# Kernel optimization log

Measured on AMD Instinct MI355X. Metric: run time of the kernel, lower is better.

Reference implementation:

```python
import jax, jax.numpy as jnp
import numpy as np

B, D, F = 64, 256, 64   # batch, in_features (window), feat_num (nodes per graph)
H, C = 4, 64            # heads, out_features per head
OUT = 64                # final out_features after concat projection
NEG_SLOPE = 0.2


def _build_edges():
    # fully connected minus self-loops within each graph, batched with node offsets
    ii = np.repeat(np.arange(F), F)
    jj = np.tile(np.arange(F), F)
    m = ii != jj
    es, ed = ii[m], jj[m]                       # [E0], E0 = F*(F-1)
    off = (np.arange(B) * F)[:, None]
    src = (es[None, :] + off).reshape(-1)       # [B*E0]
    dst = (ed[None, :] + off).reshape(-1)
    return jnp.asarray(src, jnp.int32), jnp.asarray(dst, jnp.int32)


def setup_inputs() -> dict:
    key = jax.random.key(0)
    ks = jax.random.split(key, 6)
    x = jax.random.normal(ks[0], (B, D, F), dtype=jnp.float32)
    s = 1.0 / np.sqrt(D)
    Wl = jax.random.normal(ks[1], (D, H * C), dtype=jnp.float32) * s
    Wr = jax.random.normal(ks[2], (D, H * C), dtype=jnp.float32) * s
    att = jax.random.normal(ks[3], (H, C), dtype=jnp.float32) * (1.0 / np.sqrt(C))
    bias = jax.random.normal(ks[4], (H * C,), dtype=jnp.float32) * 0.02
    Wlin = jax.random.normal(ks[5], (OUT, H * C), dtype=jnp.float32) * (1.0 / np.sqrt(H * C))
    src, dst = _build_edges()
    return {"x": x, "Wl": Wl, "Wr": Wr, "att": att, "bias": bias, "Wlin": Wlin,
            "src": src, "dst": dst}


def reference(x, Wl, Wr, att, bias, Wlin, src, dst):
    N = B * F
    xn = x.transpose(0, 2, 1).reshape(N, D)              # [N, D] node features
    xl = (xn @ Wl).reshape(N, H, C)                      # source transform
    xr = (xn @ Wr).reshape(N, H, C)                      # target transform
    # GATv2 edge scores: a^T LeakyReLU(xl[src] + xr[dst])
    e = jnp.einsum('ehc,hc->eh',
                   jax.nn.leaky_relu(xl[src] + xr[dst], NEG_SLOPE), att)  # [E, H]
    # segment softmax over incoming edges of each destination node
    emax = jax.ops.segment_max(e, dst, num_segments=N)   # [N, H]
    ee = jnp.exp(e - emax[dst])
    denom = jax.ops.segment_sum(ee, dst, num_segments=N)
    alpha = ee / denom[dst]                              # [E, H]
    # weighted scatter-aggregate of source messages
    agg = jax.ops.segment_sum(alpha[:, :, None] * xl[src], dst, num_segments=N)  # [N, H, C]
    out = agg.reshape(N, H * C) + bias
    out = out @ Wlin.T                                   # concat -> OUT projection
    return out.reshape(B, F, OUT).transpose(0, 2, 1)     # [B, OUT, F]
```

## Files before the change

### kernel.cpp

```cpp
#include <hip/hip_runtime.h>
#include <math.h>

#define B_   64
#define D_   256
#define F_   64
#define H_   4
#define C_   64
#define OUT_ 64
#define HC   256
#define N_   4096

typedef __attribute__((ext_vector_type(8)))  short bf16x8;
typedef __attribute__((ext_vector_type(16))) float f32x16;

static __device__ __forceinline__ unsigned short f2bf(float f) {
    unsigned int u = __float_as_uint(f);
    u += 0x7FFFu + ((u >> 16) & 1u);
    return (unsigned short)(u >> 16);
}
static __device__ __forceinline__ float bf2f(unsigned short h) {
    return __uint_as_float(((unsigned int)h) << 16);
}

#define GLDS(g, l) __builtin_amdgcn_global_load_lds(                         \
    (const __attribute__((address_space(1))) unsigned int*)(g),              \
    (__attribute__((address_space(3))) unsigned int*)(l), 16, 0, 0)

__global__ __launch_bounds__(256) void p0_split(
    const float* __restrict__ x, const float* __restrict__ Wl,
    const float* __restrict__ Wr,
    unsigned short* __restrict__ AThi, unsigned short* __restrict__ ATlo,
    unsigned short* __restrict__ WThi, unsigned short* __restrict__ WTlo,
    float* __restrict__ outz)
{
    __shared__ float T[128 * 65];
    const int t = threadIdx.x, blk = blockIdx.x;

    if (blk >= 144) {
        const int zb = blk - 144;
        float4* dst = (float4*)(outz + (size_t)zb * 16384);
        const float4 z = make_float4(0.f, 0.f, 0.f, 0.f);
        #pragma unroll
        for (int i = 0; i < 16; ++i) dst[i * 256 + t] = z;
        return;
    }

    const float* src; int sstride, k0, rowbase;
    unsigned short *Dhi, *Dlo;
    if (blk < 128) {
        int b = blk >> 1, kq = blk & 1;
        src = x + (size_t)b * (D_ * F_) + (size_t)(kq * 128) * F_;
        sstride = F_; k0 = kq * 128; rowbase = b * 64;
        Dhi = AThi; Dlo = ATlo;
    } else {
        int wi = blk - 128;
        int wsel = wi >> 3, rr = wi & 7, jc = rr >> 1, kq = rr & 1;
        src = (wsel ? Wr : Wl) + (size_t)(kq * 128) * HC + jc * 64;
        sstride = HC; k0 = kq * 128; rowbase = wsel * 256 + jc * 64;
        Dhi = WThi; Dlo = WTlo;
    }
    #pragma unroll
    for (int r = 0; r < 8; ++r) {
        int idx = r * 256 + t;
        int kk = idx >> 4, c4 = (idx & 15) * 4;
        float4 v = *(const float4*)&src[(size_t)kk * sstride + c4];
        T[kk * 65 + c4 + 0] = v.x;
        T[kk * 65 + c4 + 1] = v.y;
        T[kk * 65 + c4 + 2] = v.z;
        T[kk * 65 + c4 + 3] = v.w;
    }
    __syncthreads();
    const int c = t & 63, kg = t >> 6;
    const int row = rowbase + c;
    for (int cc = 0; cc < 4; ++cc) {
        int cg   = (k0 >> 3) + kg * 4 + cc;
        int phys = cg ^ (row & 7);
        unsigned int ph[4], pl[4];
        #pragma unroll
        for (int j = 0; j < 4; ++j) {
            float v0 = T[(kg * 32 + cc * 8 + 2 * j + 0) * 65 + c];
            float v1 = T[(kg * 32 + cc * 8 + 2 * j + 1) * 65 + c];
            unsigned short h0 = f2bf(v0), h1 = f2bf(v1);
            unsigned short l0 = f2bf(v0 - bf2f(h0)), l1 = f2bf(v1 - bf2f(h1));
            ph[j] = (unsigned int)h0 | ((unsigned int)h1 << 16);
            pl[j] = (unsigned int)l0 | ((unsigned int)l1 << 16);
        }
        *(uint4*)&Dhi[(size_t)row * 256 + phys * 8] = make_uint4(ph[0], ph[1], ph[2], ph[3]);
        *(uint4*)&Dlo[(size_t)row * 256 + phys * 8] = make_uint4(pl[0], pl[1], pl[2], pl[3]);
    }
}

__global__ __launch_bounds__(512, 2) void fused(
    const unsigned short* __restrict__ AThi, const unsigned short* __restrict__ ATlo,
    const unsigned short* __restrict__ WThi, const unsigned short* __restrict__ WTlo,
    const float* __restrict__ att, const float* __restrict__ bias,
    const float* __restrict__ Wlin, float* __restrict__ out)
{
    __shared__ __align__(16) char smem[98304];
    unsigned short* Ah = (unsigned short*)smem;
    unsigned short* Al = Ah + 64 * 128;
    unsigned short* Bh = Al + 64 * 128;
    unsigned short* Bl = Bh + 128 * 128;
    float* XL   = (float*)smem;
    float* XR   = XL + 64 * 68;
    float* ATe  = XR + 64 * 68;
    float* SUMD = ATe + 64 * 65;
    float* AGG  = SUMD + 64;
    float* WC   = AGG + 64 * 65;

    const int t = threadIdx.x;
    const int h = blockIdx.x, b = blockIdx.y;
    const int lane = t & 63, wid = t >> 6;
    const int wm = wid & 1, wn = wid >> 1;
    const int kg = lane >> 5, m = lane & 31;

    f32x16 acc = {};
    for (int kt = 0; kt < 2; ++kt) {
        for (int i = 0; i < 12; ++i) {
            int q = wid * 12 + i;
            const unsigned short* P; unsigned short* Lb; int li;
            if (q < 16)      { P = AThi; Lb = Ah; li = q; }
            else if (q < 32) { P = ATlo; Lb = Al; li = q - 16; }
            else if (q < 64) { P = WThi; Lb = Bh; li = q - 32; }
            else             { P = WTlo; Lb = Bl; li = q - 64; }
            int gi = li * 64 + lane;
            int row = gi >> 4, cl = gi & 15;
            int prow;
            if (q < 32) prow = b * 64 + row;
            else        prow = (row < 64) ? (h * 64 + row) : (256 + h * 64 + row - 64);
            GLDS(P + (size_t)prow * 256 + (size_t)(kt * 16 + cl) * 8, Lb + li * 512);
        }
        __syncthreads();

        const int rA = wm * 32 + m;
        const int rB = wn * 32 + m;
        #pragma unroll
        for (int s = 0; s < 8; ++s) {
            int pA = (2 * s + kg) ^ (rA & 7);
            bf16x8 ah = *(const bf16x8*)&Ah[rA * 128 + pA * 8];
            bf16x8 al = *(const bf16x8*)&Al[rA * 128 + pA * 8];
            int pB = (2 * s + kg) ^ (rB & 7);
            bf16x8 bh = *(const bf16x8*)&Bh[rB * 128 + pB * 8];
            bf16x8 bl = *(const bf16x8*)&Bl[rB * 128 + pB * 8];
            acc = __builtin_amdgcn_mfma_f32_32x32x16_bf16(ah, bh, acc, 0, 0, 0);
            acc = __builtin_amdgcn_mfma_f32_32x32x16_bf16(ah, bl, acc, 0, 0, 0);
            acc = __builtin_amdgcn_mfma_f32_32x32x16_bf16(al, bh, acc, 0, 0, 0);
        }
        __syncthreads();
    }

    {
        float* dst = (wn < 2) ? XL : XR;
        const int cdst = (wn & 1) * 32 + m;
        #pragma unroll
        for (int reg = 0; reg < 16; ++reg) {
            int crow = (reg & 3) + 8 * (reg >> 2) + 4 * kg;
            dst[(wm * 32 + crow) * 68 + cdst] = acc[reg];
        }
    }
    {
        int o = t >> 3, cl0 = (t & 7) * 8;
        const float4* srcw = (const float4*)&Wlin[(size_t)o * HC + h * 64 + cl0];
        *(float4*)&WC[o * 64 + cl0]     = srcw[0];
        *(float4*)&WC[o * 64 + cl0 + 4] = srcw[1];
    }
    __syncthreads();

    const float* attp = att + h * 64;
    float attr[64];
    #pragma unroll
    for (int c = 0; c < 64; ++c) attr[c] = attp[c];

    float xlr[64];
    #pragma unroll
    for (int c4 = 0; c4 < 64; c4 += 4) {
        float4 v = *(float4*)&XL[lane * 68 + c4];
        xlr[c4] = v.x; xlr[c4 + 1] = v.y; xlr[c4 + 2] = v.z; xlr[c4 + 3] = v.w;
    }
    float AL;
    {
        float a0 = 0.f, a1 = 0.f, a2 = 0.f, a3 = 0.f;
        #pragma unroll
        for (int c = 0; c < 64; c += 4) {
            a0 = fmaf(attr[c + 0], xlr[c + 0], a0);
            a1 = fmaf(attr[c + 1], xlr[c + 1], a1);
            a2 = fmaf(attr[c + 2], xlr[c + 2], a2);
            a3 = fmaf(attr[c + 3], xlr[c + 3], a3);
        }
        AL = (a0 + a1) + (a2 + a3);
    }

    #pragma unroll
    for (int dd = 0; dd < 8; ++dd) {
        int d = wid * 8 + dd;
        float s0 = 0.f, s1 = 0.f, s2 = 0.f, s3 = 0.f;
        #pragma unroll
        for (int c4 = 0; c4 < 64; c4 += 4) {
            float4 xr4 = *(float4*)&XR[d * 68 + c4];
            s0 = fmaf(attr[c4 + 0], fabsf(xlr[c4 + 0] + xr4.x), s0);
            s1 = fmaf(attr[c4 + 1], fabsf(xlr[c4 + 1] + xr4.y), s1);
            s2 = fmaf(attr[c4 + 2], fabsf(xlr[c4 + 2] + xr4.z), s2);
            s3 = fmaf(attr[c4 + 3], fabsf(xlr[c4 + 3] + xr4.w), s3);
        }
        float Sabs = (s0 + s1) + (s2 + s3);
        float T = fmaf(0.4f, Sabs, 0.6f * AL);
        if (lane == d) T = -1e30f;
        float e = __expf(T);
        float ssum = e;
        #pragma unroll
        for (int off = 32; off >= 1; off >>= 1)
            ssum += __shfl_xor(ssum, off, 64);
        ATe[lane * 65 + d] = e;
        if (lane == 0) SUMD[d] = ssum;
    }
    __syncthreads();

    {
        const int c0 = wid * 8;
        const float inv = 1.0f / SUMD[lane];
        float a8[8];
        #pragma unroll
        for (int i = 0; i < 8; ++i) a8[i] = 0.f;
        for (int s = 0; s < 64; ++s) {
            float a = ATe[s * 65 + lane];
            float4 v0 = *(float4*)&XL[s * 68 + c0];
            float4 v1 = *(float4*)&XL[s * 68 + c0 + 4];
            a8[0] = fmaf(a, v0.x, a8[0]); a8[1] = fmaf(a, v0.y, a8[1]);
            a8[2] = fmaf(a, v0.z, a8[2]); a8[3] = fmaf(a, v0.w, a8[3]);
            a8[4] = fmaf(a, v1.x, a8[4]); a8[5] = fmaf(a, v1.y, a8[5]);
            a8[6] = fmaf(a, v1.z, a8[6]); a8[7] = fmaf(a, v1.w, a8[7]);
        }
        const float* bp = bias + h * 64 + c0;
        #pragma unroll
        for (int j = 0; j < 8; ++j)
            AGG[lane * 65 + c0 + j] = fmaf(a8[j], inv, bp[j]);
    }
    __syncthreads();

    {
        float pacc[8];
        #pragma unroll
        for (int i = 0; i < 8; ++i) pacc[i] = 0.f;
        for (int cl = 0; cl < 64; ++cl) {
            float a = AGG[lane * 65 + cl];
            #pragma unroll
            for (int i = 0; i < 8; ++i)
                pacc[i] = fmaf(a, WC[(wid * 8 + i) * 64 + cl], pacc[i]);
        }
        float* op = out + (size_t)b * (OUT_ * F_) + lane;
        #pragma unroll
        for (int i = 0; i < 8; ++i)
            atomicAdd(op + (size_t)(wid * 8 + i) * F_, pacc[i]);
    }
}

extern "C" void kernel_launch(void* const* d_in, const int* in_sizes, int n_in,
                              void* d_out, int out_size, void* d_ws, size_t ws_size,
                              hipStream_t stream)
{
    const float* x    = (const float*)d_in[0];
    const float* Wl   = (const float*)d_in[1];
    const float* Wr   = (const float*)d_in[2];
    const float* att  = (const float*)d_in[3];
    const float* bias = (const float*)d_in[4];
    const float* Wlin = (const float*)d_in[5];

    unsigned short* AThi = (unsigned short*)d_ws;
    unsigned short* ATlo = AThi + (size_t)N_ * HC;
    unsigned short* WThi = ATlo + (size_t)N_ * HC;
    unsigned short* WTlo = WThi + (size_t)512 * HC;
    float* out = (float*)d_out;

    p0_split<<<dim3(160), 256, 0, stream>>>(x, Wl, Wr, AThi, ATlo, WThi, WTlo, out);
    fused<<<dim3(H_, B_), 512, 0, stream>>>(AThi, ATlo, WThi, WTlo,
                                            att, bias, Wlin, out);
}
```

Measured before the change: 32.99 us.

## Fuse bf16 split into main kernel and zero output via cooperative grid sync

```diff
diff --git a/kernel.cpp b/kernel.cpp
--- a/kernel.cpp
+++ b/kernel.cpp
@@ -1,5 +1,8 @@
 #include <hip/hip_runtime.h>
+#include <hip/hip_cooperative_groups.h>
 #include <math.h>
+
+namespace cg = cooperative_groups;
 
 #define B_   64
 #define D_   256
@@ -22,85 +25,19 @@
     return __uint_as_float(((unsigned int)h) << 16);
 }
 
-#define GLDS(g, l) __builtin_amdgcn_global_load_lds(                         \
-    (const __attribute__((address_space(1))) unsigned int*)(g),              \
-    (__attribute__((address_space(3))) unsigned int*)(l), 16, 0, 0)
-
-__global__ __launch_bounds__(256) void p0_split(
+template <bool COOP>
+__global__ __launch_bounds__(512, 2) void fused_kernel(
     const float* __restrict__ x, const float* __restrict__ Wl,
-    const float* __restrict__ Wr,
-    unsigned short* __restrict__ AThi, unsigned short* __restrict__ ATlo,
-    unsigned short* __restrict__ WThi, unsigned short* __restrict__ WTlo,
-    float* __restrict__ outz)
+    const float* __restrict__ Wr, const float* __restrict__ att,
+    const float* __restrict__ bias, const float* __restrict__ Wlin,
+    float* __restrict__ out)
 {
-    __shared__ float T[128 * 65];
-    const int t = threadIdx.x, blk = blockIdx.x;
-
-    if (blk >= 144) {
-        const int zb = blk - 144;
-        float4* dst = (float4*)(outz + (size_t)zb * 16384);
-        const float4 z = make_float4(0.f, 0.f, 0.f, 0.f);
-        #pragma unroll
-        for (int i = 0; i < 16; ++i) dst[i * 256 + t] = z;
-        return;
-    }
-
-    const float* src; int sstride, k0, rowbase;
-    unsigned short *Dhi, *Dlo;
-    if (blk < 128) {
-        int b = blk >> 1, kq = blk & 1;
-        src = x + (size_t)b * (D_ * F_) + (size_t)(kq * 128) * F_;
-        sstride = F_; k0 = kq * 128; rowbase = b * 64;
-        Dhi = AThi; Dlo = ATlo;
-    } else {
-        int wi = blk - 128;
-        int wsel = wi >> 3, rr = wi & 7, jc = rr >> 1, kq = rr & 1;
-        src = (wsel ? Wr : Wl) + (size_t)(kq * 128) * HC + jc * 64;
-        sstride = HC; k0 = kq * 128; rowbase = wsel * 256 + jc * 64;
-        Dhi = WThi; Dlo = WTlo;
-    }
-    #pragma unroll
-    for (int r = 0; r < 8; ++r) {
-        int idx = r * 256 + t;
-        int kk = idx >> 4, c4 = (idx & 15) * 4;
-        float4 v = *(const float4*)&src[(size_t)kk * sstride + c4];
-        T[kk * 65 + c4 + 0] = v.x;
-        T[kk * 65 + c4 + 1] = v.y;
-        T[kk * 65 + c4 + 2] = v.z;
-        T[kk * 65 + c4 + 3] = v.w;
-    }
-    __syncthreads();
-    const int c = t & 63, kg = t >> 6;
-    const int row = rowbase + c;
-    for (int cc = 0; cc < 4; ++cc) {
-        int cg   = (k0 >> 3) + kg * 4 + cc;
-        int phys = cg ^ (row & 7);
-        unsigned int ph[4], pl[4];
-        #pragma unroll
-        for (int j = 0; j < 4; ++j) {
-            float v0 = T[(kg * 32 + cc * 8 + 2 * j + 0) * 65 + c];
-            float v1 = T[(kg * 32 + cc * 8 + 2 * j + 1) * 65 + c];
-            unsigned short h0 = f2bf(v0), h1 = f2bf(v1);
-            unsigned short l0 = f2bf(v0 - bf2f(h0)), l1 = f2bf(v1 - bf2f(h1));
-            ph[j] = (unsigned int)h0 | ((unsigned int)h1 << 16);
-            pl[j] = (unsigned int)l0 | ((unsigned int)l1 << 16);
-        }
-        *(uint4*)&Dhi[(size_t)row * 256 + phys * 8] = make_uint4(ph[0], ph[1], ph[2], ph[3]);
-        *(uint4*)&Dlo[(size_t)row * 256 + phys * 8] = make_uint4(pl[0], pl[1], pl[2], pl[3]);
-    }
-}
-
-__global__ __launch_bounds__(512, 2) void fused(
-    const unsigned short* __restrict__ AThi, const unsigned short* __restrict__ ATlo,
-    const unsigned short* __restrict__ WThi, const unsigned short* __restrict__ WTlo,
-    const float* __restrict__ att, const float* __restrict__ bias,
-    const float* __restrict__ Wlin, float* __restrict__ out)
-{
-    __shared__ __align__(16) char smem[98304];
+    __shared__ __align__(16) char smem[131584];
     unsigned short* Ah = (unsigned short*)smem;
     unsigned short* Al = Ah + 64 * 128;
     unsigned short* Bh = Al + 64 * 128;
     unsigned short* Bl = Bh + 128 * 128;
+    float* T    = (float*)(smem + 98304);
     float* XL   = (float*)smem;
     float* XR   = XL + 64 * 68;
     float* ATe  = XR + 64 * 68;
@@ -114,23 +51,56 @@
     const int wm = wid & 1, wn = wid >> 1;
     const int kg = lane >> 5, m = lane & 31;
 
+    if constexpr (COOP) {
+        const int bid = b * 4 + h;
+        *((float2*)out + (size_t)bid * 512 + t) = make_float2(0.f, 0.f);
+        cg::this_grid().sync();
+    }
+
     f32x16 acc = {};
     for (int kt = 0; kt < 2; ++kt) {
-        for (int i = 0; i < 12; ++i) {
-            int q = wid * 12 + i;
-            const unsigned short* P; unsigned short* Lb; int li;
-            if (q < 16)      { P = AThi; Lb = Ah; li = q; }
-            else if (q < 32) { P = ATlo; Lb = Al; li = q - 16; }
-            else if (q < 64) { P = WThi; Lb = Bh; li = q - 32; }
-            else             { P = WTlo; Lb = Bl; li = q - 64; }
-            int gi = li * 64 + lane;
-            int row = gi >> 4, cl = gi & 15;
-            int prow;
-            if (q < 32) prow = b * 64 + row;
-            else        prow = (row < 64) ? (h * 64 + row) : (256 + h * 64 + row - 64);
-            GLDS(P + (size_t)prow * 256 + (size_t)(kt * 16 + cl) * 8, Lb + li * 512);
-        }
-        __syncthreads();
+        #pragma unroll 1
+        for (int sub = 0; sub < 3; ++sub) {
+            const float* src; int sstride;
+            if (sub == 0) { src = x + (size_t)b * (D_ * F_) + (size_t)(kt * 128) * F_; sstride = F_; }
+            else          { src = ((sub == 1) ? Wl : Wr) + (size_t)(kt * 128) * HC + h * 64; sstride = HC; }
+            #pragma unroll
+            for (int r = 0; r < 4; ++r) {
+                int idx = r * 512 + t;
+                int kk = idx >> 4, c4 = (idx & 15) * 4;
+                float4 v = *(const float4*)&src[(size_t)kk * sstride + c4];
+                T[kk * 65 + c4 + 0] = v.x;
+                T[kk * 65 + c4 + 1] = v.y;
+                T[kk * 65 + c4 + 2] = v.z;
+                T[kk * 65 + c4 + 3] = v.w;
+            }
+            __syncthreads();
+            {
+                const int col = t & 63;
+                const int kgr = t >> 6;
+                unsigned short* Dh = (sub == 0) ? Ah : Bh;
+                unsigned short* Dl = (sub == 0) ? Al : Bl;
+                const int drow = col + ((sub == 2) ? 64 : 0);
+                #pragma unroll
+                for (int cc = 0; cc < 2; ++cc) {
+                    int chunk = kgr * 2 + cc;
+                    int phys  = chunk ^ (drow & 7);
+                    unsigned int ph[4], pl[4];
+                    #pragma unroll
+                    for (int j = 0; j < 4; ++j) {
+                        float v0 = T[(chunk * 8 + 2 * j + 0) * 65 + col];
+                        float v1 = T[(chunk * 8 + 2 * j + 1) * 65 + col];
+                        unsigned short h0 = f2bf(v0), h1 = f2bf(v1);
+                        unsigned short l0 = f2bf(v0 - bf2f(h0)), l1 = f2bf(v1 - bf2f(h1));
+                        ph[j] = (unsigned int)h0 | ((unsigned int)h1 << 16);
+                        pl[j] = (unsigned int)l0 | ((unsigned int)l1 << 16);
+                    }
+                    *(uint4*)&Dh[drow * 128 + phys * 8] = make_uint4(ph[0], ph[1], ph[2], ph[3]);
+                    *(uint4*)&Dl[drow * 128 + phys * 8] = make_uint4(pl[0], pl[1], pl[2], pl[3]);
+                }
+            }
+            __syncthreads();
+        }
 
         const int rA = wm * 32 + m;
         const int rB = wn * 32 + m;
@@ -146,8 +116,8 @@
             acc = __builtin_amdgcn_mfma_f32_32x32x16_bf16(ah, bl, acc, 0, 0, 0);
             acc = __builtin_amdgcn_mfma_f32_32x32x16_bf16(al, bh, acc, 0, 0, 0);
         }
-        __syncthreads();
-    }
+    }
+    __syncthreads();
 
     {
         float* dst = (wn < 2) ? XL : XR;
@@ -203,9 +173,9 @@
             s3 = fmaf(attr[c4 + 3], fabsf(xlr[c4 + 3] + xr4.w), s3);
         }
         float Sabs = (s0 + s1) + (s2 + s3);
-        float T = fmaf(0.4f, Sabs, 0.6f * AL);
-        if (lane == d) T = -1e30f;
-        float e = __expf(T);
+        float Tv = fmaf(0.4f, Sabs, 0.6f * AL);
+        if (lane == d) Tv = -1e30f;
+        float e = __expf(Tv);
         float ssum = e;
         #pragma unroll
         for (int off = 32; off >= 1; off >>= 1)
@@ -264,14 +234,17 @@
     const float* att  = (const float*)d_in[3];
     const float* bias = (const float*)d_in[4];
     const float* Wlin = (const float*)d_in[5];
-
-    unsigned short* AThi = (unsigned short*)d_ws;
-    unsigned short* ATlo = AThi + (size_t)N_ * HC;
-    unsigned short* WThi = ATlo + (size_t)N_ * HC;
-    unsigned short* WTlo = WThi + (size_t)512 * HC;
     float* out = (float*)d_out;
 
-    p0_split<<<dim3(160), 256, 0, stream>>>(x, Wl, Wr, AThi, ATlo, WThi, WTlo, out);
-    fused<<<dim3(H_, B_), 512, 0, stream>>>(AThi, ATlo, WThi, WTlo,
-                                            att, bias, Wlin, out);
-}
+    void* args[] = { (void*)&x, (void*)&Wl, (void*)&Wr, (void*)&att,
+                     (void*)&bias, (void*)&Wlin, (void*)&out };
+    hipError_t err = hipLaunchCooperativeKernel(
+        (const void*)&fused_kernel<true>, dim3(H_, B_), dim3(512),
+        args, 0, stream);
+    if (err != hipSuccess) {
+        (void)hipGetLastError();
+        hipMemsetAsync(out, 0, (size_t)B_ * OUT_ * F_ * sizeof(float), stream);
+        fused_kernel<false><<<dim3(H_, B_), 512, 0, stream>>>(
+            x, Wl, Wr, att, bias, Wlin, out);
+    }
+}
```

Measured after the change: 62.82 us. 90.4% more time.
